# Kernel tuning notes

Hardware: AMD Instinct MI355X
Metric: run time of the kernel (lower is better)

## Reference

```python
import jax, jax.numpy as jnp
import numpy as np

PAD = 1
STRIDE = (1, 1)
TEMPERATURE = 1.0


def setup_inputs() -> dict:
    key = jax.random.key(0)
    ks = jax.random.split(key, 5)
    x = jax.random.normal(ks[0], (16, 256, 56, 56), dtype=jnp.float32)
    kernels = jax.random.normal(ks[1], (8, 256, 256, 3, 3), dtype=jnp.float32)
    w1 = jax.random.normal(ks[2], (256, 64), dtype=jnp.float32) * 0.0625
    b1 = jnp.zeros((64,), dtype=jnp.float32)
    w2 = jax.random.normal(ks[3], (64, 8), dtype=jnp.float32) * 0.125
    b2 = jnp.zeros((8,), dtype=jnp.float32)
    return {"x": x, "kernels": kernels, "w1": w1, "b1": b1, "w2": w2, "b2": b2}


def _forward(x, kernels, w1, b1, w2, b2):
    # Attention: global average pool -> MLP -> softmax over kernels
    pooled = jnp.mean(x, axis=(2, 3))                      # [B, C]
    h = jax.nn.relu(pooled @ w1 + b1)                      # [B, H]
    scores = h @ w2 + b2                                   # [B, K]
    alphas = jax.nn.softmax(scores / TEMPERATURE, axis=-1) # [B, K]

    # Per-sample mixed kernels: [B, O, I, kh, kw]
    weighted = jnp.einsum('bk,koihw->boihw', alphas, kernels)

    # Per-sample conv2d (groups=1), vectorized over batch
    def conv_one(xi, wi):
        return jax.lax.conv_general_dilated(
            xi[None], wi, STRIDE, [(PAD, PAD), (PAD, PAD)],
            dimension_numbers=('NCHW', 'OIHW', 'NCHW'))[0]

    return jax.vmap(conv_one)(x, weighted)                 # [B, O, H, W]


def reference(x, kernels, w1, b1, w2, b2):
    return _forward(x, kernels, w1, b1, w2, b2)
```

## Files before the change

kernel.cpp:

```cpp
#include <hip/hip_runtime.h>
#include <hip/hip_bf16.h>
#include <stdint.h>

typedef __attribute__((ext_vector_type(8))) short bf16x8;
typedef __attribute__((ext_vector_type(4))) float f32x4;

#define BATCH 16
#define CH    256
#define HW    56
#define HWHW  3136
#define NK    8

#define XPT_BYTES   30408704ul
#define WK_BYTES    18874368ul
#define POOL_BYTES  16384ul
#define ALPHA_BYTES 512ul

__device__ __forceinline__ void gl_lds16(const void* g, void* l) {
    __builtin_amdgcn_global_load_lds((const __attribute__((address_space(1))) uint32_t*)g,
                                     (__attribute__((address_space(3))) uint32_t*)l, 16, 0, 0);
}

__global__ void pool_kernel(const float* __restrict__ x, float* __restrict__ pooled) {
    int bc = blockIdx.x;
    const float* p = x + (size_t)bc * HWHW;
    float s = 0.f;
    for (int t = threadIdx.x; t < HWHW; t += 256) s += p[t];
    for (int off = 32; off; off >>= 1) s += __shfl_down(s, off);
    __shared__ float ws4[4];
    if ((threadIdx.x & 63) == 0) ws4[threadIdx.x >> 6] = s;
    __syncthreads();
    if (threadIdx.x == 0)
        pooled[bc] = (ws4[0] + ws4[1] + ws4[2] + ws4[3]) * (1.0f / 3136.0f);
}

__global__ void xpose_kernel(const float* __restrict__ x, __hip_bfloat16* __restrict__ xp) {
    int ic4 = blockIdx.x;
    int y   = blockIdx.y;
    int b   = blockIdx.z;
    __shared__ __hip_bfloat16 t[64][57];
    int lane = threadIdx.x & 63;
    int quad = threadIdx.x >> 6;
    const float* src = x + ((size_t)(b * CH + ic4 * 64) * HW + y) * HW;
    for (int ii = quad; ii < 64; ii += 4) {
        if (lane < 56) t[ii][lane] = __float2bfloat16(src[(size_t)ii * HWHW + lane]);
    }
    __syncthreads();
    __hip_bfloat16* dst = xp + ((size_t)(b * 58 + (y + 1)) * 64) * 256 + (size_t)ic4 * 64;
    for (int xx = quad; xx < 56; xx += 4) {
        dst[(size_t)(xx + 1) * 256 + lane] = t[lane][xx];
    }
}

__global__ void mlp_kernel(const float* __restrict__ pooled,
                           const float* __restrict__ w1, const float* __restrict__ b1,
                           const float* __restrict__ w2, const float* __restrict__ b2,
                           float* __restrict__ alphas) {
    __shared__ float hs[16][64];
    __shared__ float sc[16][8];
    int t = threadIdx.x;
    for (int idx = t; idx < 16 * 64; idx += 256) {
        int b = idx >> 6, j = idx & 63;
        float acc = b1[j];
        const float* pb = pooled + b * 256;
        for (int c = 0; c < 256; ++c) acc += pb[c] * w1[c * 64 + j];
        hs[b][j] = fmaxf(acc, 0.0f);
    }
    __syncthreads();
    if (t < 128) {
        int b = t >> 3, k = t & 7;
        float acc = b2[k];
        for (int j = 0; j < 64; ++j) acc += hs[b][j] * w2[j * 8 + k];
        sc[b][k] = acc;
    }
    __syncthreads();
    if (t < 16) {
        float m = -1e30f;
        for (int k = 0; k < 8; ++k) m = fmaxf(m, sc[t][k]);
        float s = 0.f, e[8];
        for (int k = 0; k < 8; ++k) { e[k] = expf(sc[t][k] - m); s += e[k]; }
        float inv = 1.0f / s;
        for (int k = 0; k < 8; ++k) alphas[t * 8 + k] = e[k] * inv;
    }
}

__global__ void wmix_kernel(const float* __restrict__ kern, const float* __restrict__ alphas,
                            __hip_bfloat16* __restrict__ wk) {
    __shared__ float al[16][8];
    int t = threadIdx.x;
    if (t < 128) al[t >> 3][t & 7] = alphas[t];
    __syncthreads();
    int idx = blockIdx.x * 256 + t;
    float kv[8][9];
    const float* kp = kern + (size_t)idx * 9;
#pragma unroll
    for (int k = 0; k < 8; ++k)
#pragma unroll
        for (int q = 0; q < 9; ++q) kv[k][q] = kp[(size_t)k * 589824 + q];
#pragma unroll 1
    for (int b = 0; b < 16; ++b) {
#pragma unroll
        for (int q = 0; q < 9; ++q) {
            float acc = 0.f;
#pragma unroll
            for (int k = 0; k < 8; ++k) acc += al[b][k] * kv[k][q];
            wk[(((size_t)(b * 9 + q) * 256) << 8) + idx] = __float2bfloat16(acc);
        }
    }
}

__global__ void __launch_bounds__(256, 2)
conv_kernel(const __hip_bfloat16* __restrict__ xpT, const __hip_bfloat16* __restrict__ wk,
            float* __restrict__ out) {
    __shared__ short lds_x[6 * 64 * 32];
    __shared__ short lds_a[128 * 32];

    const int tid   = threadIdx.x;
    const int lane  = tid & 63;
    const int g     = lane >> 4;
    const int l15   = lane & 15;
    const int w     = tid >> 6;
    const int wm    = w >> 1;
    const int wn    = w & 1;
    const int w64   = tid & ~63;

    const int mtile = blockIdx.x;
    const int y0    = blockIdx.y * 4;
    const int b     = blockIdx.z;

    int cellb[7], c3[7], rr[7], cc[7];
#pragma unroll
    for (int fn = 0; fn < 7; ++fn) {
        int n = wn * 112 + fn * 16 + l15;
        int r = n / 56, c = n % 56;
        rr[fn] = r; cc[fn] = c;
        cellb[fn] = r * 64 + c;
        c3[fn] = c & 3;
    }
    const int aoff = (wm * 64 + l15) * 64 + ((g ^ (l15 & 3)) << 4);

    f32x4 acc[4][7];
#pragma unroll
    for (int fm = 0; fm < 4; ++fm)
#pragma unroll
        for (int fn = 0; fn < 7; ++fn) acc[fm][fn] = (f32x4){0.f, 0.f, 0.f, 0.f};

    const size_t xb = ((size_t)b * 58 + y0) * 64 * 256;

    for (int ci = 0; ci < 8; ++ci) {
#pragma unroll
        for (int it = 0; it < 6; ++it) {
            int idx  = it * 256 + tid;
            int slot = idx & 3, cell = idx >> 2;
            int c = cell & 63, r = cell >> 6;
            int tslot = slot ^ (c & 3);
            const __hip_bfloat16* src = xpT + xb + ((size_t)(r * 64 + c)) * 256 + ci * 32 + tslot * 8;
            gl_lds16(src, (char*)lds_x + (it * 256 + w64) * 16);
        }
        for (int kk = 0; kk < 9; ++kk) {
            const int kh = kk / 3, kw = kk % 3;
            const size_t wbase = (((size_t)(b * 9 + kk) * 256 + mtile * 128)) << 8;
#pragma unroll
            for (int it = 0; it < 2; ++it) {
                int idx  = it * 256 + tid;
                int slot = idx & 3, o = idx >> 2;
                int tslot = slot ^ (o & 3);
                const __hip_bfloat16* src = wk + wbase + ((size_t)o << 8) + ci * 32 + tslot * 8;
                gl_lds16(src, (char*)lds_a + (it * 256 + w64) * 16);
            }
            __syncthreads();

            bf16x8 af[4];
#pragma unroll
            for (int fm = 0; fm < 4; ++fm)
                af[fm] = *(const bf16x8*)((const char*)lds_a + aoff + fm * 1024);
#pragma unroll
            for (int fn = 0; fn < 7; ++fn) {
                int cell = cellb[fn] + kh * 64 + kw;
                int slot = g ^ ((c3[fn] + kw) & 3);
                bf16x8 bfv = *(const bf16x8*)((const char*)lds_x + cell * 64 + (slot << 4));
#pragma unroll
                for (int fm = 0; fm < 4; ++fm)
                    acc[fm][fn] = __builtin_amdgcn_mfma_f32_16x16x32_bf16(af[fm], bfv, acc[fm][fn], 0, 0, 0);
            }
            __syncthreads();
        }
    }

    const int mbase = mtile * 128 + wm * 64;
#pragma unroll
    for (int fm = 0; fm < 4; ++fm)
#pragma unroll
        for (int fn = 0; fn < 7; ++fn) {
            int o = mbase + fm * 16 + 4 * g;
            float* op = out + (((size_t)b * 256 + o) * 56 + (y0 + rr[fn])) * 56 + cc[fn];
#pragma unroll
            for (int r = 0; r < 4; ++r) op[(size_t)r * HWHW] = acc[fm][fn][r];
        }
}

extern "C" void kernel_launch(void* const* d_in, const int* in_sizes, int n_in,
                              void* d_out, int out_size, void* d_ws, size_t ws_size,
                              hipStream_t stream) {
    const float* x    = (const float*)d_in[0];
    const float* kern = (const float*)d_in[1];
    const float* w1   = (const float*)d_in[2];
    const float* b1   = (const float*)d_in[3];
    const float* w2   = (const float*)d_in[4];
    const float* b2   = (const float*)d_in[5];
    float* out = (float*)d_out;

    char* wsp = (char*)d_ws;
    __hip_bfloat16* xpT    = (__hip_bfloat16*)wsp;
    __hip_bfloat16* wkbuf  = (__hip_bfloat16*)(wsp + XPT_BYTES);
    float*          pooled = (float*)(wsp + XPT_BYTES + WK_BYTES);
    float*          alphas = (float*)(wsp + XPT_BYTES + WK_BYTES + POOL_BYTES);

    hipMemsetAsync(xpT, 0, XPT_BYTES, stream);

    pool_kernel<<<dim3(BATCH * CH), dim3(256), 0, stream>>>(x, pooled);
    xpose_kernel<<<dim3(4, 56, 16), dim3(256), 0, stream>>>(x, xpT);
    mlp_kernel<<<dim3(1), dim3(256), 0, stream>>>(pooled, w1, b1, w2, b2, alphas);
    wmix_kernel<<<dim3(256), dim3(256), 0, stream>>>(kern, alphas, wkbuf);
    conv_kernel<<<dim3(2, 14, 16), dim3(256), 0, stream>>>(xpT, wkbuf, out);
}
```

Measured before the change: 281.8 us.

## Fuse pool with transpose, double-buffer conv LDS staging, swizzle block order

Merges the pooling and bf16 transpose passes into one kernel that reads x once with float4 loads, accumulates the channel means with atomics, and zeroes only the padding border instead of memsetting the whole buffer. The conv kernel now double-buffers its input and weight LDS tiles, prefetching the next (ci, kk) stage while MFMAs run on the current one, which halves the barriers per step. Conv blocks are launched on a flat grid with a swizzled index so that blocks sharing a batch's weights are scheduled apart. The extra LDS doubles the shared-memory footprint, and pooling now sums bf16-rounded values, which slightly changes the numerics.

```diff
diff --git a/kernel.cpp b/kernel.cpp
--- a/kernel.cpp
+++ b/kernel.cpp
@@ -21,34 +21,67 @@
                                      (__attribute__((address_space(3))) uint32_t*)l, 16, 0, 0);
 }
 
-__global__ void pool_kernel(const float* __restrict__ x, float* __restrict__ pooled) {
-    int bc = blockIdx.x;
-    const float* p = x + (size_t)bc * HWHW;
-    float s = 0.f;
-    for (int t = threadIdx.x; t < HWHW; t += 256) s += p[t];
-    for (int off = 32; off; off >>= 1) s += __shfl_down(s, off);
-    __shared__ float ws4[4];
-    if ((threadIdx.x & 63) == 0) ws4[threadIdx.x >> 6] = s;
-    __syncthreads();
-    if (threadIdx.x == 0)
-        pooled[bc] = (ws4[0] + ws4[1] + ws4[2] + ws4[3]) * (1.0f / 3136.0f);
-}
-
-__global__ void xpose_kernel(const float* __restrict__ x, __hip_bfloat16* __restrict__ xp) {
-    int ic4 = blockIdx.x;
-    int y   = blockIdx.y;
-    int b   = blockIdx.z;
-    __shared__ __hip_bfloat16 t[64][57];
-    int lane = threadIdx.x & 63;
-    int quad = threadIdx.x >> 6;
-    const float* src = x + ((size_t)(b * CH + ic4 * 64) * HW + y) * HW;
-    for (int ii = quad; ii < 64; ii += 4) {
-        if (lane < 56) t[ii][lane] = __float2bfloat16(src[(size_t)ii * HWHW + lane]);
-    }
-    __syncthreads();
-    __hip_bfloat16* dst = xp + ((size_t)(b * 58 + (y + 1)) * 64) * 256 + (size_t)ic4 * 64;
-    for (int xx = quad; xx < 56; xx += 4) {
-        dst[(size_t)(xx + 1) * 256 + lane] = t[lane][xx];
+__device__ __forceinline__ float bf16bits_to_f32(short h) {
+    return __uint_as_float(((uint32_t)(uint16_t)h) << 16);
+}
+
+__global__ void __launch_bounds__(256, 2)
+xpose_pool_kernel(const float* __restrict__ x, __hip_bfloat16* __restrict__ xp,
+                  float* __restrict__ pooled) {
+    __shared__ short tile[2 * 56 * 256];
+    const int tid = threadIdx.x;
+    const int ys  = blockIdx.x;
+    const int b   = blockIdx.y;
+    const int y0  = ys * 2;
+
+    const float* xb = x + (size_t)b * CH * HWHW + (size_t)y0 * HW;
+    for (int it = 0; it < 28; ++it) {
+        int idx = it * 256 + tid;
+        int ch  = idx / 28;
+        int xi  = idx - ch * 28;
+        int r   = xi / 14;
+        int x4  = (xi - r * 14) * 4;
+        const float4 v = *(const float4*)(xb + (size_t)ch * HWHW + r * HW + x4);
+        const float* vf = (const float*)&v;
+#pragma unroll
+        for (int j = 0; j < 4; ++j) {
+            __hip_bfloat16 h = __float2bfloat16(vf[j]);
+            tile[(r * 56 + x4 + j) * 256 + (ch ^ (((x4 & 7) | j) << 3))] = *(const short*)&h;
+        }
+    }
+    __syncthreads();
+
+    {
+        float s = 0.f;
+        const int ch = tid;
+        for (int r = 0; r < 2; ++r)
+            for (int xx = 0; xx < 56; ++xx)
+                s += bf16bits_to_f32(tile[(r * 56 + xx) * 256 + (ch ^ ((xx & 7) << 3))]);
+        atomicAdd(&pooled[b * 256 + ch], s * (1.0f / 3136.0f));
+    }
+
+    __hip_bfloat16* dst0 = xp + ((size_t)(b * 58 + y0 + 1) * 64 + 1) * 256;
+    for (int it = 0; it < 14; ++it) {
+        int idx = it * 256 + tid;
+        int ch0 = (idx & 31) * 8;
+        int pos = idx >> 5;
+        int r = pos / 56, xx = pos - (pos / 56) * 56;
+        bf16x8 vv = *(const bf16x8*)&tile[(r * 56 + xx) * 256 + (ch0 ^ ((xx & 7) << 3))];
+        *(bf16x8*)(dst0 + ((size_t)(r * 64 + xx)) * 256 + ch0) = vv;
+    }
+
+    bf16x8 z = {};
+    if (tid < 128) {
+        int r   = tid >> 6;
+        int c2  = (tid >> 5) & 1;
+        int ch0 = (tid & 31) * 8;
+        *(bf16x8*)(xp + ((size_t)(b * 58 + y0 + 1 + r) * 64 + (c2 ? 57 : 0)) * 256 + ch0) = z;
+    }
+    if (ys == 0 || ys == 27) {
+        int p = (ys == 0) ? 0 : 57;
+        __hip_bfloat16* rowp = xp + (size_t)(b * 58 + p) * 64 * 256;
+        for (int it = tid; it < 2048; it += 256)
+            *(bf16x8*)(rowp + (size_t)it * 8) = z;
     }
 }
 
@@ -112,8 +145,8 @@
 __global__ void __launch_bounds__(256, 2)
 conv_kernel(const __hip_bfloat16* __restrict__ xpT, const __hip_bfloat16* __restrict__ wk,
             float* __restrict__ out) {
-    __shared__ short lds_x[6 * 64 * 32];
-    __shared__ short lds_a[128 * 32];
+    __shared__ short lds_x[2][6 * 64 * 32];
+    __shared__ short lds_a[2][128 * 32];
 
     const int tid   = threadIdx.x;
     const int lane  = tid & 63;
@@ -124,9 +157,12 @@
     const int wn    = w & 1;
     const int w64   = tid & ~63;
 
-    const int mtile = blockIdx.x;
-    const int y0    = blockIdx.y * 4;
-    const int b     = blockIdx.z;
+    const int flat  = blockIdx.x;
+    const int swzid = (flat & 7) * 56 + (flat >> 3);
+    const int b     = swzid / 28;
+    const int rem   = swzid - b * 28;
+    const int mtile = rem & 1;
+    const int y0    = (rem >> 1) * 4;
 
     int cellb[7], c3[7], rr[7], cc[7];
 #pragma unroll
@@ -147,44 +183,66 @@
 
     const size_t xb = ((size_t)b * 58 + y0) * 64 * 256;
 
-    for (int ci = 0; ci < 8; ++ci) {
-#pragma unroll
-        for (int it = 0; it < 6; ++it) {
-            int idx  = it * 256 + tid;
-            int slot = idx & 3, cell = idx >> 2;
-            int c = cell & 63, r = cell >> 6;
-            int tslot = slot ^ (c & 3);
-            const __hip_bfloat16* src = xpT + xb + ((size_t)(r * 64 + c)) * 256 + ci * 32 + tslot * 8;
-            gl_lds16(src, (char*)lds_x + (it * 256 + w64) * 16);
-        }
-        for (int kk = 0; kk < 9; ++kk) {
-            const int kh = kk / 3, kw = kk % 3;
-            const size_t wbase = (((size_t)(b * 9 + kk) * 256 + mtile * 128)) << 8;
-#pragma unroll
-            for (int it = 0; it < 2; ++it) {
-                int idx  = it * 256 + tid;
-                int slot = idx & 3, o = idx >> 2;
-                int tslot = slot ^ (o & 3);
-                const __hip_bfloat16* src = wk + wbase + ((size_t)o << 8) + ci * 32 + tslot * 8;
-                gl_lds16(src, (char*)lds_a + (it * 256 + w64) * 16);
-            }
-            __syncthreads();
-
-            bf16x8 af[4];
+#define STAGE_X(CI, BUF)                                                            \
+    do {                                                                            \
+        _Pragma("unroll")                                                           \
+        for (int it = 0; it < 6; ++it) {                                            \
+            int idx = it * 256 + tid;                                               \
+            int slot = idx & 3, cell = idx >> 2;                                    \
+            int c = cell & 63;                                                      \
+            int tslot = slot ^ (c & 3);                                             \
+            const __hip_bfloat16* src = xpT + xb + (size_t)cell * 256 + (CI) * 32 + tslot * 8; \
+            gl_lds16(src, (char*)lds_x[BUF] + (it * 256 + w64) * 16);               \
+        }                                                                           \
+    } while (0)
+
+#define STAGE_A(CI, KK, BUF)                                                        \
+    do {                                                                            \
+        const size_t wbase = ((size_t)((b * 9 + (KK)) * 256 + mtile * 128)) << 8;   \
+        _Pragma("unroll")                                                           \
+        for (int it = 0; it < 2; ++it) {                                            \
+            int idx = it * 256 + tid;                                               \
+            int slot = idx & 3, o = idx >> 2;                                       \
+            int tslot = slot ^ (o & 3);                                             \
+            const __hip_bfloat16* src = wk + wbase + ((size_t)o << 8) + (CI) * 32 + tslot * 8; \
+            gl_lds16(src, (char*)lds_a[BUF] + (it * 256 + w64) * 16);               \
+        }                                                                           \
+    } while (0)
+
+    STAGE_X(0, 0);
+    STAGE_A(0, 0, 0);
+    __syncthreads();
+
+    int cab = 0, cxb = 0;
+    int kk = 0, kh = 0, kw = 0, ci = 0;
+#pragma unroll 1
+    for (int s = 0; s < 72; ++s) {
+        int nkk = kk + 1, nci = ci;
+        if (nkk == 9) { nkk = 0; ++nci; }
+        if (s < 71) {
+            STAGE_A(nci, nkk, cab ^ 1);
+            if (kk == 8) STAGE_X(nci, cxb ^ 1);
+        }
+
+        bf16x8 af[4];
+#pragma unroll
+        for (int fm = 0; fm < 4; ++fm)
+            af[fm] = *(const bf16x8*)((const char*)lds_a[cab] + aoff + fm * 1024);
+#pragma unroll
+        for (int fn = 0; fn < 7; ++fn) {
+            int cell = cellb[fn] + kh * 64 + kw;
+            int slot = g ^ ((c3[fn] + kw) & 3);
+            bf16x8 bfv = *(const bf16x8*)((const char*)lds_x[cxb] + cell * 64 + (slot << 4));
 #pragma unroll
             for (int fm = 0; fm < 4; ++fm)
-                af[fm] = *(const bf16x8*)((const char*)lds_a + aoff + fm * 1024);
-#pragma unroll
-            for (int fn = 0; fn < 7; ++fn) {
-                int cell = cellb[fn] + kh * 64 + kw;
-                int slot = g ^ ((c3[fn] + kw) & 3);
-                bf16x8 bfv = *(const bf16x8*)((const char*)lds_x + cell * 64 + (slot << 4));
-#pragma unroll
-                for (int fm = 0; fm < 4; ++fm)
-                    acc[fm][fn] = __builtin_amdgcn_mfma_f32_16x16x32_bf16(af[fm], bfv, acc[fm][fn], 0, 0, 0);
-            }
-            __syncthreads();
-        }
+                acc[fm][fn] = __builtin_amdgcn_mfma_f32_16x16x32_bf16(af[fm], bfv, acc[fm][fn], 0, 0, 0);
+        }
+
+        __syncthreads();
+        cab ^= 1;
+        if (kk == 8) cxb ^= 1;
+        kk = nkk; ci = nci;
+        if (++kw == 3) { kw = 0; if (++kh == 3) kh = 0; }
     }
 
     const int mbase = mtile * 128 + wm * 64;
@@ -197,6 +255,8 @@
 #pragma unroll
             for (int r = 0; r < 4; ++r) op[(size_t)r * HWHW] = acc[fm][fn][r];
         }
+#undef STAGE_X
+#undef STAGE_A
 }
 
 extern "C" void kernel_launch(void* const* d_in, const int* in_sizes, int n_in,
@@ -216,11 +276,10 @@
     float*          pooled = (float*)(wsp + XPT_BYTES + WK_BYTES);
     float*          alphas = (float*)(wsp + XPT_BYTES + WK_BYTES + POOL_BYTES);
 
-    hipMemsetAsync(xpT, 0, XPT_BYTES, stream);
-
-    pool_kernel<<<dim3(BATCH * CH), dim3(256), 0, stream>>>(x, pooled);
-    xpose_kernel<<<dim3(4, 56, 16), dim3(256), 0, stream>>>(x, xpT);
+    hipMemsetAsync(pooled, 0, POOL_BYTES, stream);
+
+    xpose_pool_kernel<<<dim3(28, 16), dim3(256), 0, stream>>>(x, xpT, pooled);
     mlp_kernel<<<dim3(1), dim3(256), 0, stream>>>(pooled, w1, b1, w2, b2, alphas);
     wmix_kernel<<<dim3(256), dim3(256), 0, stream>>>(kern, alphas, wkbuf);
-    conv_kernel<<<dim3(2, 14, 16), dim3(256), 0, stream>>>(xpT, wkbuf, out);
-}
+    conv_kernel<<<dim3(448), dim3(256), 0, stream>>>(xpT, wkbuf, out);
+}
```

After: 251.0 us. 10.9% less time.
